# Kernel tuning notes

Measured on AMD Instinct MI355X. Metric: run time of the kernel, lower is better.

Reference implementation:

```python
import jax, jax.numpy as jnp
import numpy as np

N, M, E, DIM, H = 50000, 50000, 640000, 128, 8
DH = DIM // H
EPS = 1e-5

def _prelu(x, alpha):
    return jnp.where(x >= 0, x, alpha * x)

def setup_inputs() -> dict:
    key0 = jax.random.key(0)
    ks = jax.random.split(key0, 12)
    s = 1.0 / np.sqrt(DIM)
    return {
        "query": jax.random.normal(ks[0], (N, DIM), jnp.float32),
        "key": jax.random.normal(ks[1], (M, DIM), jnp.float32),
        "value": jax.random.normal(ks[2], (M, DIM), jnp.float32),
        "query_idx": jax.random.randint(ks[3], (E,), 0, N),
        "key_idx": jax.random.randint(ks[4], (E,), 0, M),
        "Wq": jax.random.normal(ks[5], (DIM, DIM), jnp.float32) * s,
        "bq": jnp.zeros((DIM,), jnp.float32),
        "Wk": jax.random.normal(ks[6], (DIM, DIM), jnp.float32) * s,
        "bk": jnp.zeros((DIM,), jnp.float32),
        "Wv": jax.random.normal(ks[7], (DIM, DIM), jnp.float32) * s,
        "bv": jnp.zeros((DIM,), jnp.float32),
        "Wp": jax.random.normal(ks[8], (DIM, DIM), jnp.float32) * s,
        "bp": jnp.zeros((DIM,), jnp.float32),
        "a": jax.random.normal(ks[9], (1, H, DH), jnp.float32) * 0.1,
        "alpha": jnp.full((1,), 0.25, jnp.float32),
        "gamma": jnp.ones((DIM,), jnp.float32),
        "beta": jnp.zeros((DIM,), jnp.float32),
    }

def reference(query, key, value, query_idx, key_idx, Wq, bq, Wk, bk, Wv, bv, Wp, bp, a, alpha, gamma, beta):
    n = query.shape[0]
    # projections (node-level, then gather per edge; linear commutes with gather)
    Qq = query @ Wq + bq            # [N, DIM]
    Kq = query @ Wk + bk            # [N, DIM] (self-attn key)
    Kk = key @ Wk + bk              # [M, DIM]
    Vq = query @ Wv + bv            # [N, DIM]
    Vv = value @ Wv + bv            # [M, DIM]
    # self-attention score per query node: [N, H, 1]
    attn_qq = (a * _prelu(Qq + Kq, alpha).reshape(n, H, DH)).sum(-1, keepdims=True)
    # per-edge additive attention score: [E, H, 1]
    e_feat = _prelu(Qq[query_idx] + Kk[key_idx], alpha)
    attn_e = (a * e_feat.reshape(-1, H, DH)).sum(-1, keepdims=True)
    # stable softmax over irregular query groups (include self)
    max_attn = jax.lax.stop_gradient(attn_qq.at[query_idx].max(attn_e))
    exp_qq = jnp.exp(attn_qq - max_attn)                 # [N, H, 1]
    exp_e = jnp.exp(attn_e - max_attn[query_idx])        # [E, H, 1]
    denom = exp_qq.at[query_idx].add(exp_e)              # [N, H, 1]
    denom = jnp.where(denom == 0, 1.0, denom)
    # weighted value scatter-sum (value_idx == key_idx)
    msg = exp_qq * Vq.reshape(n, H, DH)
    msg = msg.at[query_idx].add(exp_e * Vv[key_idx].reshape(-1, H, DH))
    out = (msg / denom).reshape(n, DIM) @ Wp + bp
    res = query + out
    mu = res.mean(-1, keepdims=True)
    var = res.var(-1, keepdims=True)
    return gamma * (res - mu) / jnp.sqrt(var + EPS) + beta
```

## Files before the change

### kernel.cpp

```cpp
#include <hip/hip_runtime.h>
#include <math.h>

#define DIM 128
#define NH 8
#define LN_EPS 1e-5f
#define NEGINF -3.0e38f

using bf16x8 = __attribute__((ext_vector_type(8))) short;
using f32x4  = __attribute__((ext_vector_type(4))) float;

__device__ __forceinline__ float prelu_f(float x, float al) { return x >= 0.f ? x : al * x; }

__device__ __forceinline__ short f2bf(float f) {
    unsigned u = __float_as_uint(f);
    unsigned r = (u + 0x7fffu + ((u >> 16) & 1u)) >> 16;
    return (short)r;
}
__device__ __forceinline__ float bflo(unsigned u) { return __uint_as_float(u << 16); }
__device__ __forceinline__ float bfhi(unsigned u) { return __uint_as_float(u & 0xffff0000u); }

__device__ __forceinline__ unsigned cvt_pk_bf16(float lo, float hi) {
    unsigned r;
    asm("v_cvt_pk_bf16_f32 %0, %1, %2" : "=v"(r) : "v"(lo), "v"(hi));
    return r;
}

__device__ __forceinline__ float swz_xor1(float x) {
    return __int_as_float(__builtin_amdgcn_ds_swizzle(__float_as_int(x), 0x041F));
}
__device__ __forceinline__ float swz_xor2(float x) {
    return __int_as_float(__builtin_amdgcn_ds_swizzle(__float_as_int(x), 0x081F));
}
__device__ __forceinline__ float swz_xor16(float x) {
    return __int_as_float(__builtin_amdgcn_ds_swizzle(__float_as_int(x), 0x401F));
}

__global__ __launch_bounds__(256) void setup_kernel(
    const float* __restrict__ W0, const float* __restrict__ W1,
    const float* __restrict__ W2, const float* __restrict__ W3,
    short* __restrict__ P0, short* __restrict__ P1,
    short* __restrict__ P2, short* __restrict__ P3,
    const int* __restrict__ qidx, int* __restrict__ counts, int E)
{
    if (blockIdx.x < 32) {
        const int id = blockIdx.x * 256 + threadIdx.x;
        const int mat = id >> 11;
        const int rem = id & 2047;
        const int ks = rem >> 9;
        const int ct = (rem >> 6) & 7;
        const int lane = rem & 63;
        const int lr = lane & 15, lg = lane >> 4;
        const float* W = mat == 0 ? W0 : mat == 1 ? W1 : mat == 2 ? W2 : W3;
        short* P = mat == 0 ? P0 : mat == 1 ? P1 : mat == 2 ? P2 : P3;
        short v[8];
        #pragma unroll
        for (int r = 0; r < 8; ++r)
            v[r] = f2bf(W[(ks * 32 + lg * 8 + r) * DIM + ct * 16 + lr]);
        *(bf16x8*)&P[(size_t)((ks * 8 + ct) * 64 + lane) * 8] = *(bf16x8*)v;
    } else {
        const int b = blockIdx.x - 32;
        for (int e = b * 256 + threadIdx.x; e < E; e += 1024 * 256)
            atomicAdd(&counts[qidx[e]], 1);
    }
}

__global__ __launch_bounds__(256) void proj_all_mfma(
    const float* __restrict__ query,
    const float* __restrict__ key, const float* __restrict__ value,
    const short* __restrict__ Wqp, const short* __restrict__ Wkp, const short* __restrict__ Wvp,
    const float* __restrict__ bq, const float* __restrict__ bk, const float* __restrict__ bv,
    const float* __restrict__ avec, const float* __restrict__ alpha_p,
    short* __restrict__ QV16, float* __restrict__ attnqq4,
    short* __restrict__ KV16, int N, int M, int nb)
{
    __shared__ unsigned lds[4][16][66];
    const int wid = threadIdx.x >> 6, lane = threadIdx.x & 63;
    const int lr = lane & 15, lg = lane >> 4;
    const bool evenlane = (lane & 1) == 0;

    if ((int)blockIdx.x < nb) {
        const int row0 = ((int)blockIdx.x * 4 + wid) * 16;
        if (row0 >= N) return;
        const int arow = row0 + lr;
        const bool rowok = arow < N;

        bf16x8 afrag[4];
        #pragma unroll
        for (int ks = 0; ks < 4; ++ks) {
            float t[8] = {0.f,0.f,0.f,0.f,0.f,0.f,0.f,0.f};
            if (rowok) {
                *(float4*)&t[0] = *(const float4*)&query[(size_t)arow * DIM + ks * 32 + lg * 8];
                *(float4*)&t[4] = *(const float4*)&query[(size_t)arow * DIM + ks * 32 + lg * 8 + 4];
            }
            union { bf16x8 v; unsigned u[4]; } a;
            a.u[0] = cvt_pk_bf16(t[0], t[1]);
            a.u[1] = cvt_pk_bf16(t[2], t[3]);
            a.u[2] = cvt_pk_bf16(t[4], t[5]);
            a.u[3] = cvt_pk_bf16(t[6], t[7]);
            afrag[ks] = a.v;
        }
        const float al = alpha_p[0];
        unsigned* qvout = (unsigned*)QV16;

        #pragma unroll 1
        for (int ct = 0; ct < 8; ++ct) {
            f32x4 aq = (f32x4)0.f, ak = (f32x4)0.f;
            #pragma unroll
            for (int ks = 0; ks < 4; ++ks) {
                const size_t bo = (size_t)((ks * 8 + ct) * 64 + lane) * 8;
                aq = __builtin_amdgcn_mfma_f32_16x16x32_bf16(afrag[ks], *(const bf16x8*)&Wqp[bo], aq, 0, 0, 0);
                ak = __builtin_amdgcn_mfma_f32_16x16x32_bf16(afrag[ks], *(const bf16x8*)&Wkp[bo], ak, 0, 0, 0);
            }
            const int col = ct * 16 + lr;
            const float bqv = bq[col], bkv = bk[col], av = avec[col];
            #pragma unroll
            for (int r = 0; r < 4; ++r) {
                const int row = lg * 4 + r;
                const float qv = aq[r] + bqv;
                const float kv = ak[r] + bkv;
                float part = av * prelu_f(qv + kv, al);
                part += swz_xor1(part);
                part += swz_xor2(part);
                const int grow = row0 + row;
                if ((lr & 3) == 0 && grow < N)
                    attnqq4[(size_t)grow * 32 + ct * 4 + (lr >> 2)] = part;
                const float qn = swz_xor1(qv);
                if (evenlane) lds[wid][row][ct * 8 + (lr >> 1)] = cvt_pk_bf16(qv, qn);
            }
        }
        #pragma unroll
        for (int rr = 0; rr < 16; ++rr) {
            const int grow = row0 + rr;
            if (grow < N) qvout[(size_t)grow * 128 + lane] = lds[wid][rr][lane];
        }

        #pragma unroll 1
        for (int ct = 0; ct < 8; ++ct) {
            f32x4 acv = (f32x4)0.f;
            #pragma unroll
            for (int ks = 0; ks < 4; ++ks) {
                const size_t bo = (size_t)((ks * 8 + ct) * 64 + lane) * 8;
                acv = __builtin_amdgcn_mfma_f32_16x16x32_bf16(afrag[ks], *(const bf16x8*)&Wvp[bo], acv, 0, 0, 0);
            }
            const int col = ct * 16 + lr;
            const float bvv = bv[col];
            #pragma unroll
            for (int r = 0; r < 4; ++r) {
                const int row = lg * 4 + r;
                const float vv = acv[r] + bvv;
                const float vn = swz_xor1(vv);
                if (evenlane) lds[wid][row][ct * 8 + (lr >> 1)] = cvt_pk_bf16(vv, vn);
            }
        }
        #pragma unroll
        for (int rr = 0; rr < 16; ++rr) {
            const int grow = row0 + rr;
            if (grow < N) qvout[(size_t)grow * 128 + 64 + lane] = lds[wid][rr][lane];
        }
    } else {
        const int row0 = (((int)blockIdx.x - nb) * 4 + wid) * 16;
        if (row0 >= M) return;
        const int arow = row0 + lr;
        const bool rowok = arow < M;
        unsigned* kvout = (unsigned*)KV16;

        {
            bf16x8 afK[4];
            #pragma unroll
            for (int ks = 0; ks < 4; ++ks) {
                float t[8] = {0.f,0.f,0.f,0.f,0.f,0.f,0.f,0.f};
                if (rowok) {
                    *(float4*)&t[0] = *(const float4*)&key[(size_t)arow * DIM + ks * 32 + lg * 8];
                    *(float4*)&t[4] = *(const float4*)&key[(size_t)arow * DIM + ks * 32 + lg * 8 + 4];
                }
                union { bf16x8 v; unsigned u[4]; } a;
                a.u[0] = cvt_pk_bf16(t[0], t[1]);
                a.u[1] = cvt_pk_bf16(t[2], t[3]);
                a.u[2] = cvt_pk_bf16(t[4], t[5]);
                a.u[3] = cvt_pk_bf16(t[6], t[7]);
                afK[ks] = a.v;
            }
            #pragma unroll 1
            for (int ct = 0; ct < 8; ++ct) {
                f32x4 ack = (f32x4)0.f;
                #pragma unroll
                for (int ks = 0; ks < 4; ++ks) {
                    const size_t bo = (size_t)((ks * 8 + ct) * 64 + lane) * 8;
                    ack = __builtin_amdgcn_mfma_f32_16x16x32_bf16(afK[ks], *(const bf16x8*)&Wkp[bo], ack, 0, 0, 0);
                }
                const int col = ct * 16 + lr;
                const float bkv = bk[col];
                #pragma unroll
                for (int r = 0; r < 4; ++r) {
                    const int row = lg * 4 + r;
                    const float kv = ack[r] + bkv;
                    const float kn = swz_xor1(kv);
                    if (evenlane) lds[wid][row][ct * 8 + (lr >> 1)] = cvt_pk_bf16(kv, kn);
                }
            }
            #pragma unroll
            for (int rr = 0; rr < 16; ++rr) {
                const int grow = row0 + rr;
                if (grow < M) kvout[(size_t)grow * 128 + lane] = lds[wid][rr][lane];
            }
        }
        {
            bf16x8 afV[4];
            #pragma unroll
            for (int ks = 0; ks < 4; ++ks) {
                float t[8] = {0.f,0.f,0.f,0.f,0.f,0.f,0.f,0.f};
                if (rowok) {
                    *(float4*)&t[0] = *(const float4*)&value[(size_t)arow * DIM + ks * 32 + lg * 8];
                    *(float4*)&t[4] = *(const float4*)&value[(size_t)arow * DIM + ks * 32 + lg * 8 + 4];
                }
                union { bf16x8 v; unsigned u[4]; } a;
                a.u[0] = cvt_pk_bf16(t[0], t[1]);
                a.u[1] = cvt_pk_bf16(t[2], t[3]);
                a.u[2] = cvt_pk_bf16(t[4], t[5]);
                a.u[3] = cvt_pk_bf16(t[6], t[7]);
                afV[ks] = a.v;
            }
            #pragma unroll 1
            for (int ct = 0; ct < 8; ++ct) {
                f32x4 acv = (f32x4)0.f;
                #pragma unroll
                for (int ks = 0; ks < 4; ++ks) {
                    const size_t bo = (size_t)((ks * 8 + ct) * 64 + lane) * 8;
                    acv = __builtin_amdgcn_mfma_f32_16x16x32_bf16(afV[ks], *(const bf16x8*)&Wvp[bo], acv, 0, 0, 0);
                }
                const int col = ct * 16 + lr;
                const float bvv = bv[col];
                #pragma unroll
                for (int r = 0; r < 4; ++r) {
                    const int row = lg * 4 + r;
                    const float vv = acv[r] + bvv;
                    const float vn = swz_xor1(vv);
                    if (evenlane) lds[wid][row][ct * 8 + (lr >> 1)] = cvt_pk_bf16(vv, vn);
                }
            }
            #pragma unroll
            for (int rr = 0; rr < 16; ++rr) {
                const int grow = row0 + rr;
                if (grow < M) kvout[(size_t)grow * 128 + 64 + lane] = lds[wid][rr][lane];
            }
        }
    }
}

__global__ __launch_bounds__(256) void scan1_kernel(const int* __restrict__ counts,
                                                    int* __restrict__ bsum, int N)
{
    __shared__ int sh[256];
    int i = blockIdx.x * 256 + threadIdx.x;
    sh[threadIdx.x] = (i < N) ? counts[i] : 0;
    __syncthreads();
    #pragma unroll
    for (int off = 128; off; off >>= 1) {
        if (threadIdx.x < off) sh[threadIdx.x] += sh[threadIdx.x + off];
        __syncthreads();
    }
    if (threadIdx.x == 0) bsum[blockIdx.x] = sh[0];
}

__global__ __launch_bounds__(256) void scan2_kernel(const int* __restrict__ bsum,
                                                    int* __restrict__ boff, int B)
{
    int t = threadIdx.x;
    if (B > 256) {
        if (t == 0) { int run = 0; for (int i = 0; i < B; ++i) { int v = bsum[i]; boff[i] = run; run += v; } }
        return;
    }
    __shared__ int sh[256];
    int v = (t < B) ? bsum[t] : 0;
    sh[t] = v;
    __syncthreads();
    for (int off = 1; off < 256; off <<= 1) {
        int x = (t >= off) ? sh[t - off] : 0;
        __syncthreads();
        sh[t] += x;
        __syncthreads();
    }
    if (t < B) boff[t] = sh[t] - v;
}

__global__ __launch_bounds__(256) void scan3_kernel(const int* __restrict__ counts,
                                                    const int* __restrict__ boff,
                                                    int* __restrict__ offsets,
                                                    int* __restrict__ cursor,
                                                    int N, int E)
{
    __shared__ int sh[256];
    int t = threadIdx.x;
    int i = blockIdx.x * 256 + t;
    int v = (i < N) ? counts[i] : 0;
    sh[t] = v;
    __syncthreads();
    for (int off = 1; off < 256; off <<= 1) {
        int x = (t >= off) ? sh[t - off] : 0;
        __syncthreads();
        sh[t] += x;
        __syncthreads();
    }
    int base = boff[blockIdx.x];
    if (i < N) {
        int o = base + sh[t] - v;
        offsets[i] = o;
        cursor[i] = o;
    }
    if (i == 0) offsets[N] = E;
}

__global__ void fill_kernel(const int* __restrict__ qidx, const int* __restrict__ kidx,
                            int* __restrict__ cursor, int* __restrict__ ksorted, int E)
{
    for (int e = blockIdx.x * blockDim.x + threadIdx.x; e < E; e += gridDim.x * blockDim.x) {
        int q = qidx[e];
        int pos = atomicAdd(&cursor[q], 1);
        ksorted[pos] = kidx[e];
    }
}

__global__ __launch_bounds__(256) void edge_agg_kernel(
    const short* __restrict__ QV16, const float* __restrict__ attnqq4,
    const short* __restrict__ KV16,
    const int* __restrict__ ksorted, const int* __restrict__ offsets,
    const float* __restrict__ avec, const float* __restrict__ alpha_p,
    short* __restrict__ msgn16, int N)
{
    const int lane = threadIdx.x & 63;
    const int wid  = threadIdx.x >> 6;
    const int half = lane >> 5;
    const int e    = (lane >> 4) & 1;
    const int sub  = lane & 15;
    const int h    = sub >> 1;

    const float al = alpha_p[0];
    const float r  = (1.f - al) / (1.f + al);
    const float s1 = (1.f + al) * 0.5f;

    float c[8];
    {
        const float4 a0 = *(const float4*)&avec[sub * 8];
        const float4 a1 = *(const float4*)&avec[sub * 8 + 4];
        c[0] = a0.x * s1; c[1] = a0.y * s1; c[2] = a0.z * s1; c[3] = a0.w * s1;
        c[4] = a1.x * s1; c[5] = a1.y * s1; c[6] = a1.z * s1; c[7] = a1.w * s1;
    }

    const int npairs = (N + 1) >> 1;
    const int wavesTotal = gridDim.x * 4;

    for (int pair = blockIdx.x * 4 + wid; pair < npairs; pair += wavesTotal) {
        const int n = pair * 2 + half;
        const bool nvalid = n < N;
        const int nn = nvalid ? n : (N - 1);

        float q[8];
        {
            unsigned qd[4];
            *(uint4*)qd = *(const uint4*)&QV16[(size_t)nn * 256 + sub * 8];
            #pragma unroll
            for (int j = 0; j < 4; ++j) { q[2*j] = bflo(qd[j]); q[2*j+1] = bfhi(qd[j]); }
        }

        float acc[8];
        float den;
        if (e == 0) {
            unsigned vdi[4];
            *(uint4*)vdi = *(const uint4*)&QV16[(size_t)nn * 256 + 128 + sub * 8];
            #pragma unroll
            for (int j = 0; j < 4; ++j) { acc[2*j] = bflo(vdi[j]); acc[2*j+1] = bfhi(vdi[j]); }
            den = 1.f;
        } else {
            #pragma unroll
            for (int d = 0; d < 8; ++d) acc[d] = 0.f;
            den = 0.f;
        }

        float m;
        {
            const float4 a4 = *(const float4*)&attnqq4[(size_t)nn * 32 + h * 4];
            m = (a4.x + a4.y) + (a4.z + a4.w);
        }

        const int p0 = nvalid ? offsets[nn] : 0;
        const int p1 = nvalid ? offsets[nn + 1] : 0;
        bool div = false;

        const int idx0 = p0 + e;
        bool v0 = idx0 < p1;
        const int ki0 = v0 ? ksorted[idx0] : 0;
        unsigned kd0[4], vd0[4];
        {
            const size_t kb = (size_t)ki0 * 256 + sub * 8;
            *(uint4*)kd0 = *(const uint4*)&KV16[kb];
            *(uint4*)vd0 = *(const uint4*)&KV16[kb + 128];
        }

        for (int it = 1; __any(v0); ++it) {
            const int nidx = p0 + it * 2 + e;
            const bool v1 = nidx < p1;
            const int ki1 = v1 ? ksorted[nidx] : 0;
            unsigned kd1[4], vd1[4];
            {
                const size_t kb = (size_t)ki1 * 256 + sub * 8;
                *(uint4*)kd1 = *(const uint4*)&KV16[kb];
                *(uint4*)vd1 = *(const uint4*)&KV16[kb + 128];
            }

            float sp = 0.f;
            #pragma unroll
            for (int j = 0; j < 4; ++j) {
                const float x0 = q[2*j]   + bflo(kd0[j]);
                const float x1 = q[2*j+1] + bfhi(kd0[j]);
                const float t0 = fmaf(r, __builtin_fabsf(x0), x0);
                const float t1 = fmaf(r, __builtin_fabsf(x1), x1);
                sp = fmaf(c[2*j], t0, sp);
                sp = fmaf(c[2*j+1], t1, sp);
            }
            const float sf = sp + swz_xor1(sp);
            const float s = v0 ? sf : NEGINF;
            const float d_ = s - m;

            if (__any(d_ > 8.f)) {
                div = true;
                const float nm = fmaxf(m, s);
                const float cc = __expf(m - nm);
                const float w = __expf(s - nm);
                den = den * cc + w;
                #pragma unroll
                for (int j = 0; j < 4; ++j) {
                    acc[2*j]   = fmaf(acc[2*j],   cc, w * bflo(vd0[j]));
                    acc[2*j+1] = fmaf(acc[2*j+1], cc, w * bfhi(vd0[j]));
                }
                m = nm;
            } else {
                const float w = __expf(d_);
                den += w;
                #pragma unroll
                for (int j = 0; j < 4; ++j) {
                    acc[2*j]   = fmaf(w, bflo(vd0[j]), acc[2*j]);
                    acc[2*j+1] = fmaf(w, bfhi(vd0[j]), acc[2*j+1]);
                }
            }

            #pragma unroll
            for (int j = 0; j < 4; ++j) { kd0[j] = kd1[j]; vd0[j] = vd1[j]; }
            v0 = v1;
        }

        if (div) {
            const float m2 = swz_xor16(m);
            const float den2 = swz_xor16(den);
            const float nm = fmaxf(m, m2);
            const float ca = __expf(m - nm);
            const float cb = __expf(m2 - nm);
            den = den * ca + den2 * cb;
            #pragma unroll
            for (int d = 0; d < 8; ++d)
                acc[d] = acc[d] * ca + swz_xor16(acc[d]) * cb;
        } else {
            den += swz_xor16(den);
            #pragma unroll
            for (int d = 0; d < 8; ++d) acc[d] += swz_xor16(acc[d]);
        }

        if (e == 0 && nvalid) {
            const float inv = 1.f / den;
            unsigned u[4];
            #pragma unroll
            for (int j = 0; j < 4; ++j)
                u[j] = cvt_pk_bf16(acc[2*j] * inv, acc[2*j+1] * inv);
            *(uint4*)&msgn16[(size_t)n * DIM + sub * 8] = *(uint4*)u;
        }
    }
}

__global__ __launch_bounds__(256) void out_ln_mfma(
    const short* __restrict__ msgn16, const short* __restrict__ Wpp,
    const float* __restrict__ bp, const float* __restrict__ query,
    const float* __restrict__ gamma, const float* __restrict__ beta,
    float* __restrict__ out, int N)
{
    __shared__ float ys[64][130];
    const int wid = threadIdx.x >> 6, lane = threadIdx.x & 63;
    const int rowbase = blockIdx.x * 64;
    const int row0 = rowbase + wid * 16;
    const int lr = lane & 15, lg = lane >> 4;

    if (row0 < N) {
        bf16x8 afrag[4];
        const int arow = row0 + lr;
        const bool rowok = arow < N;
        #pragma unroll
        for (int ks = 0; ks < 4; ++ks) {
            if (rowok)
                afrag[ks] = *(const bf16x8*)&msgn16[(size_t)arow * DIM + ks * 32 + lg * 8];
            else {
                bf16x8 z;
                #pragma unroll
                for (int j = 0; j < 8; ++j) z[j] = 0;
                afrag[ks] = z;
            }
        }
        #pragma unroll 1
        for (int ct = 0; ct < 8; ++ct) {
            f32x4 acc = (f32x4)0.f;
            #pragma unroll
            for (int ks = 0; ks < 4; ++ks) {
                const size_t bo = (size_t)((ks * 8 + ct) * 64 + lane) * 8;
                acc = __builtin_amdgcn_mfma_f32_16x16x32_bf16(afrag[ks], *(const bf16x8*)&Wpp[bo], acc, 0, 0, 0);
            }
            const int col = ct * 16 + lr;
            const float bpv = bp[col];
            #pragma unroll
            for (int r = 0; r < 4; ++r)
                ys[wid * 16 + lg * 4 + r][col] = acc[r] + bpv;
        }
    }
    __syncthreads();

    for (int rr = 0; rr < 16; ++rr) {
        const int r = wid * 16 + rr;
        const int grow = rowbase + r;
        if (grow >= N) break;
        const float y1 = ys[r][lane], y2 = ys[r][lane + 64];
        const float q1 = query[(size_t)grow * DIM + lane];
        const float q2 = query[(size_t)grow * DIM + lane + 64];
        const float r1 = y1 + q1, r2 = y2 + q2;
        float s = r1 + r2;
        float ss = r1 * r1 + r2 * r2;
        #pragma unroll
        for (int off = 32; off; off >>= 1) {
            s += __shfl_xor(s, off);
            ss += __shfl_xor(ss, off);
        }
        const float mu = s * (1.f / DIM);
        const float var = ss * (1.f / DIM) - mu * mu;
        const float rstd = rsqrtf(var + LN_EPS);
        out[(size_t)grow * DIM + lane] = gamma[lane] * (r1 - mu) * rstd + beta[lane];
        out[(size_t)grow * DIM + lane + 64] = gamma[lane + 64] * (r2 - mu) * rstd + beta[lane + 64];
    }
}

extern "C" void kernel_launch(void* const* d_in, const int* in_sizes, int n_in,
                              void* d_out, int out_size, void* d_ws, size_t ws_size,
                              hipStream_t stream) {
    const float* query = (const float*)d_in[0];
    const float* key   = (const float*)d_in[1];
    const float* value = (const float*)d_in[2];
    const int* query_idx = (const int*)d_in[3];
    const int* key_idx   = (const int*)d_in[4];
    const float* Wq = (const float*)d_in[5];
    const float* bq = (const float*)d_in[6];
    const float* Wk = (const float*)d_in[7];
    const float* bk = (const float*)d_in[8];
    const float* Wv = (const float*)d_in[9];
    const float* bv = (const float*)d_in[10];
    const float* Wp = (const float*)d_in[11];
    const float* bp = (const float*)d_in[12];
    const float* avec  = (const float*)d_in[13];
    const float* alpha = (const float*)d_in[14];
    const float* gamma = (const float*)d_in[15];
    const float* beta  = (const float*)d_in[16];
    float* out = (float*)d_out;

    const int N = in_sizes[0] / DIM;
    const int M = in_sizes[1] / DIM;
    const int E = in_sizes[3];

    float* f = (float*)d_ws;
    float* attnqq4 = f; f += (size_t)N * 32;
    short* sp = (short*)f;
    short* QV16 = sp;   sp += (size_t)N * 256;
    short* KV16 = sp;   sp += (size_t)M * 256;
    short* msgn16 = sp; sp += (size_t)N * DIM;
    short* Wqp = sp;    sp += DIM * DIM;
    short* Wkp = sp;    sp += DIM * DIM;
    short* Wvp = sp;    sp += DIM * DIM;
    short* Wpp = sp;    sp += DIM * DIM;
    int* ip = (int*)(((size_t)sp + 15) & ~(size_t)15);
    int* counts  = ip;  ip += N;
    int* offsets = ip;  ip += N + 1;
    int* cursor  = ip;  ip += N;
    int* bsum    = ip;  ip += 4096;
    int* boff    = ip;  ip += 4096;
    int* ksorted = ip;  ip += E;

    const int B = (N + 255) / 256;
    const int nb = (N + 63) / 64;
    const int mb = (M + 63) / 64;

    hipMemsetAsync(counts, 0, (size_t)N * sizeof(int), stream);

    setup_kernel<<<1056, 256, 0, stream>>>(Wq, Wk, Wv, Wp, Wqp, Wkp, Wvp, Wpp,
                                           query_idx, counts, E);

    scan1_kernel<<<B, 256, 0, stream>>>(counts, bsum, N);
    scan2_kernel<<<1, 256, 0, stream>>>(bsum, boff, B);
    scan3_kernel<<<B, 256, 0, stream>>>(counts, boff, offsets, cursor, N, E);
    fill_kernel<<<1024, 256, 0, stream>>>(query_idx, key_idx, cursor, ksorted, E);

    proj_all_mfma<<<nb + mb, 256, 0, stream>>>(
        query, key, value, Wqp, Wkp, Wvp, bq, bk, bv, avec, alpha,
        QV16, attnqq4, KV16, N, M, nb);

    edge_agg_kernel<<<2048, 256, 0, stream>>>(
        QV16, attnqq4, KV16, ksorted, offsets, avec, alpha, msgn16, N);

    out_ln_mfma<<<(N + 63) / 64, 256, 0, stream>>>(
        msgn16, Wpp, bp, query, gamma, beta, out, N);
}
```

Measured before the change: 214.8 us.

## Process one query node per wave with four edge lanes, unroll MFMA column loops

The edge-aggregation kernel now gives each wave a single query node and splits its edges across four 16-lane groups instead of two nodes with two groups each. The per-lane partial softmax states are then merged with an extra cross-half reduction round using a lane shuffle. Separately, the MFMA column-tile loops in the projection and output kernels are unrolled by two to expose more independent work per iteration. More edge lanes per node shortens the serial edge chain for high-degree nodes but wastes lanes when degree is low (average about 13), and the unrolling adds register pressure.

```diff
diff --git a/kernel.cpp b/kernel.cpp
--- a/kernel.cpp
+++ b/kernel.cpp
@@ -33,6 +33,9 @@
 }
 __device__ __forceinline__ float swz_xor16(float x) {
     return __int_as_float(__builtin_amdgcn_ds_swizzle(__float_as_int(x), 0x401F));
+}
+__device__ __forceinline__ float swz_xor32(float x) {
+    return __shfl_xor(x, 32);
 }
 
 __global__ __launch_bounds__(256) void setup_kernel(
@@ -102,7 +105,7 @@
         const float al = alpha_p[0];
         unsigned* qvout = (unsigned*)QV16;
 
-        #pragma unroll 1
+        #pragma unroll 2
         for (int ct = 0; ct < 8; ++ct) {
             f32x4 aq = (f32x4)0.f, ak = (f32x4)0.f;
             #pragma unroll
@@ -134,7 +137,7 @@
             if (grow < N) qvout[(size_t)grow * 128 + lane] = lds[wid][rr][lane];
         }
 
-        #pragma unroll 1
+        #pragma unroll 2
         for (int ct = 0; ct < 8; ++ct) {
             f32x4 acv = (f32x4)0.f;
             #pragma unroll
@@ -180,7 +183,7 @@
                 a.u[3] = cvt_pk_bf16(t[6], t[7]);
                 afK[ks] = a.v;
             }
-            #pragma unroll 1
+            #pragma unroll 2
             for (int ct = 0; ct < 8; ++ct) {
                 f32x4 ack = (f32x4)0.f;
                 #pragma unroll
@@ -220,7 +223,7 @@
                 a.u[3] = cvt_pk_bf16(t[6], t[7]);
                 afV[ks] = a.v;
             }
-            #pragma unroll 1
+            #pragma unroll 2
             for (int ct = 0; ct < 8; ++ct) {
                 f32x4 acv = (f32x4)0.f;
                 #pragma unroll
@@ -329,8 +332,7 @@
 {
     const int lane = threadIdx.x & 63;
     const int wid  = threadIdx.x >> 6;
-    const int half = lane >> 5;
-    const int e    = (lane >> 4) & 1;
+    const int e    = lane >> 4;
     const int sub  = lane & 15;
     const int h    = sub >> 1;
 
@@ -346,18 +348,13 @@
         c[4] = a1.x * s1; c[5] = a1.y * s1; c[6] = a1.z * s1; c[7] = a1.w * s1;
     }
 
-    const int npairs = (N + 1) >> 1;
     const int wavesTotal = gridDim.x * 4;
 
-    for (int pair = blockIdx.x * 4 + wid; pair < npairs; pair += wavesTotal) {
-        const int n = pair * 2 + half;
-        const bool nvalid = n < N;
-        const int nn = nvalid ? n : (N - 1);
-
+    for (int n = blockIdx.x * 4 + wid; n < N; n += wavesTotal) {
         float q[8];
         {
             unsigned qd[4];
-            *(uint4*)qd = *(const uint4*)&QV16[(size_t)nn * 256 + sub * 8];
+            *(uint4*)qd = *(const uint4*)&QV16[(size_t)n * 256 + sub * 8];
             #pragma unroll
             for (int j = 0; j < 4; ++j) { q[2*j] = bflo(qd[j]); q[2*j+1] = bfhi(qd[j]); }
         }
@@ -366,7 +363,7 @@
         float den;
         if (e == 0) {
             unsigned vdi[4];
-            *(uint4*)vdi = *(const uint4*)&QV16[(size_t)nn * 256 + 128 + sub * 8];
+            *(uint4*)vdi = *(const uint4*)&QV16[(size_t)n * 256 + 128 + sub * 8];
             #pragma unroll
             for (int j = 0; j < 4; ++j) { acc[2*j] = bflo(vdi[j]); acc[2*j+1] = bfhi(vdi[j]); }
             den = 1.f;
@@ -378,12 +375,12 @@
 
         float m;
         {
-            const float4 a4 = *(const float4*)&attnqq4[(size_t)nn * 32 + h * 4];
+            const float4 a4 = *(const float4*)&attnqq4[(size_t)n * 32 + h * 4];
             m = (a4.x + a4.y) + (a4.z + a4.w);
         }
 
-        const int p0 = nvalid ? offsets[nn] : 0;
-        const int p1 = nvalid ? offsets[nn + 1] : 0;
+        const int p0 = offsets[n];
+        const int p1 = offsets[n + 1];
         bool div = false;
 
         const int idx0 = p0 + e;
@@ -397,7 +394,7 @@
         }
 
         for (int it = 1; __any(v0); ++it) {
-            const int nidx = p0 + it * 2 + e;
+            const int nidx = p0 + it * 4 + e;
             const bool v1 = nidx < p1;
             const int ki1 = v1 ? ksorted[nidx] : 0;
             unsigned kd1[4], vd1[4];
@@ -448,23 +445,36 @@
             v0 = v1;
         }
 
+        #define MERGE_ROUND(SWZ)                                    \
+            {                                                       \
+                const float m2 = SWZ(m);                            \
+                const float den2 = SWZ(den);                        \
+                const float nm = fmaxf(m, m2);                      \
+                const float ca = __expf(m - nm);                    \
+                const float cb = __expf(m2 - nm);                   \
+                den = den * ca + den2 * cb;                         \
+                _Pragma("unroll")                                   \
+                for (int d = 0; d < 8; ++d)                         \
+                    acc[d] = acc[d] * ca + SWZ(acc[d]) * cb;        \
+                m = nm;                                             \
+            }
+        #define SUM_ROUND(SWZ)                                      \
+            {                                                       \
+                den += SWZ(den);                                    \
+                _Pragma("unroll")                                   \
+                for (int d = 0; d < 8; ++d) acc[d] += SWZ(acc[d]);  \
+            }
         if (div) {
-            const float m2 = swz_xor16(m);
-            const float den2 = swz_xor16(den);
-            const float nm = fmaxf(m, m2);
-            const float ca = __expf(m - nm);
-            const float cb = __expf(m2 - nm);
-            den = den * ca + den2 * cb;
-            #pragma unroll
-            for (int d = 0; d < 8; ++d)
-                acc[d] = acc[d] * ca + swz_xor16(acc[d]) * cb;
+            MERGE_ROUND(swz_xor16);
+            MERGE_ROUND(swz_xor32);
         } else {
-            den += swz_xor16(den);
-            #pragma unroll
-            for (int d = 0; d < 8; ++d) acc[d] += swz_xor16(acc[d]);
-        }
-
-        if (e == 0 && nvalid) {
+            SUM_ROUND(swz_xor16);
+            SUM_ROUND(swz_xor32);
+        }
+        #undef MERGE_ROUND
+        #undef SUM_ROUND
+
+        if (e == 0) {
             const float inv = 1.f / den;
             unsigned u[4];
             #pragma unroll
@@ -502,7 +512,7 @@
                 afrag[ks] = z;
             }
         }
-        #pragma unroll 1
+        #pragma unroll 2
         for (int ct = 0; ct < 8; ++ct) {
             f32x4 acc = (f32x4)0.f;
             #pragma unroll
```

New measurement: 214.9 us. No clear change (+0.0%).
